# Performance work log

Hardware: AMD Instinct MI355X
Metric: run time of the kernel (lower is better)

The kernel has to match this reference:

```python
import jax, jax.numpy as jnp
import numpy as np

B, S, D, H = 4, 2048, 1024, 16
DK = D // H
NEG = -1e9


def setup_inputs() -> dict:
    key = jax.random.key(0)
    k1, k2, k3, k4 = jax.random.split(key, 4)
    x = jax.random.normal(k1, (B, S, D), dtype=jnp.float32)
    # seq_lens sorted descending; first entry must equal max_len (as the torch
    # code uses seq_lens[0] as max_len for the mask)
    sl = jax.random.randint(k2, (B,), S // 2, S + 1)
    sl = jnp.sort(sl)[::-1].at[0].set(S).astype(jnp.int64)
    # params of the output projection nn.Linear(d_m, d_m)
    lim = 1.0 / np.sqrt(D)
    W = jax.random.uniform(k3, (D, D), minval=-lim, maxval=lim, dtype=jnp.float32)
    b = jax.random.uniform(k4, (D,), minval=-lim, maxval=lim, dtype=jnp.float32)
    return {"x": x, "seq_lens": sl, "W": W, "b": b}


def reference(x, seq_lens, W, b):
    # key padding mask: (B, 1, 1, S) -> True where key position is valid
    valid = jnp.arange(S)[None, :] < seq_lens[:, None]          # (B, S)
    mask = valid[:, None, None, :]                              # (B, 1, 1, S)
    # split heads: (B, S, D) -> (B, H, S, DK)
    xh = x.reshape(B, S, H, DK).transpose(0, 2, 1, 3)
    scores = jnp.einsum("bhqd,bhkd->bhqk", xh, xh) / jnp.sqrt(jnp.float32(DK))
    scores = jnp.where(mask, scores, NEG)
    attn = jax.nn.softmax(scores, axis=-1)                      # (B, H, S, S)
    # dropout(0.1) omitted (eval-mode deterministic reference)
    ctx = jnp.einsum("bhqk,bhkd->bhqd", attn, xh)
    ctx = ctx.transpose(0, 2, 1, 3).reshape(B, S, D)
    out = ctx @ W.T + b                                         # (B, S, D)
    return (jnp.sum(out, axis=1), attn)
```

## Files before the change

### kernel.cpp

```cpp
#include <hip/hip_runtime.h>

#define S_  2048
#define D_  1024
#define H_  16
#define B_  4

typedef __attribute__((ext_vector_type(8))) short short8;
typedef __attribute__((ext_vector_type(4))) float f32x4;

__device__ __forceinline__ unsigned short f2bf(float f) {
  unsigned int u = __float_as_uint(f);
  u += 0x7fffu + ((u >> 16) & 1u);
  return (unsigned short)(u >> 16);
}
__device__ __forceinline__ unsigned int pack2(float a, float b) {
  return (unsigned int)f2bf(a) | ((unsigned int)f2bf(b) << 16);
}
__device__ __forceinline__ float h2f(unsigned int u, int shft) {
  unsigned short hs = (unsigned short)(u >> shft);
  return (float)__builtin_bit_cast(_Float16, hs);
}

#define SCL   0.18033688011112042f
#define EBIAS 12.0f

__global__ __launch_bounds__(256) void xcvt(const float* __restrict__ x,
                                            unsigned short* __restrict__ xh) {
  const int n = blockIdx.x;
  const int bh = n >> 5, chunk = n & 31;
  const int b = bh >> 4, h = bh & 15;
  const int r = threadIdx.x >> 2, cg = threadIdx.x & 3;
  const int srow = chunk * 64 + r;
  const float* src = x + ((size_t)b * S_ + srow) * D_ + h * 64 + cg * 16;
  float4 v0 = ((const float4*)src)[0];
  float4 v1 = ((const float4*)src)[1];
  float4 v2 = ((const float4*)src)[2];
  float4 v3 = ((const float4*)src)[3];
  uint4 w0, w1;
  w0.x = pack2(v0.x, v0.y); w0.y = pack2(v0.z, v0.w);
  w0.z = pack2(v1.x, v1.y); w0.w = pack2(v1.z, v1.w);
  w1.x = pack2(v2.x, v2.y); w1.y = pack2(v2.z, v2.w);
  w1.z = pack2(v3.x, v3.y); w1.w = pack2(v3.z, v3.w);
  unsigned short* dst = xh + ((size_t)bh * S_ + srow) * 64 + cg * 16;
  *(uint4*)dst = w0;
  *(uint4*)(dst + 8) = w1;
}

__global__ __launch_bounds__(256, 2) void attn_fused(
    const unsigned short* __restrict__ xh, const int* __restrict__ sl32,
    float* __restrict__ attn, unsigned int* __restrict__ cpart)
{
  __shared__ __align__(16) unsigned short kbuf[2][64 * 64];
  __shared__ __align__(16) unsigned int ebuf[8][2048];
  float* wbuf   = (float*)&kbuf[0][0];
  float* invbuf = (float*)&kbuf[1][0];

  const int n    = blockIdx.x;
  const int xcd  = n & 7;
  const int slot = n >> 3;
  const int bh   = (slot >> 7) * 8 + xcd;
  const int qt   = slot & 127;
  const int b    = bh >> 4;
  const int tid  = threadIdx.x;
  const int wv   = tid >> 6;
  const int lane = tid & 63;
  const int lo   = lane & 15;
  const int g    = lane >> 4;

  const bool is64 = (sl32[1] == 0);
  const int seqlen = is64 ? sl32[2 * b] : sl32[b];

  const unsigned short* xk = xh + (size_t)bh * S_ * 64;

  short8 aq0 = *(const short8*)(xk + (size_t)(qt * 16 + lo) * 64 + g * 8);
  short8 aq1 = *(const short8*)(xk + (size_t)(qt * 16 + lo) * 64 + g * 8 + 32);

  const int sr = tid >> 2, up = tid & 3;
  uint4 pf0, pf1;
  auto prefetch = [&](int c) {
    const uint4* src = (const uint4*)(xk + (size_t)(c * 64 + sr) * 64) + up * 2;
    pf0 = src[0]; pf1 = src[1];
  };
  auto commit = [&](unsigned short* dst) {
    uint4* d = (uint4*)&dst[sr * 64];
    const int sw = sr & 7;
    d[(up * 2) ^ sw]     = pf0;
    d[(up * 2 + 1) ^ sw] = pf1;
  };

  float rsum[4] = {0.f, 0.f, 0.f, 0.f};
  prefetch(0);
  commit(kbuf[0]);
  __syncthreads();
  const int lk = wv * 16 + lo;
  const int cs = g ^ (lk & 7);
  const int sA = ((g * 2) & 6) << 2;
  for (int c = 0; c < 32; ++c) {
    if (c < 31) prefetch(c + 1);
    const unsigned short* kb = kbuf[c & 1];
    short8 b0 = *(const short8*)&kb[lk * 64 + cs * 8];
    short8 b1 = *(const short8*)&kb[lk * 64 + (cs ^ 4) * 8];
    f32x4 acc = {0.f, 0.f, 0.f, 0.f};
    acc = __builtin_amdgcn_mfma_f32_16x16x32_bf16(aq0, b0, acc, 0, 0, 0);
    acc = __builtin_amdgcn_mfma_f32_16x16x32_bf16(aq1, b1, acc, 0, 0, 0);
    const int kg = c * 64 + lk;
    const bool valid = kg < seqlen;
    float e0 = valid ? exp2f(acc[0] * SCL - EBIAS) : 0.f;
    float e1 = valid ? exp2f(acc[1] * SCL - EBIAS) : 0.f;
    float e2 = valid ? exp2f(acc[2] * SCL - EBIAS) : 0.f;
    float e3 = valid ? exp2f(acc[3] * SCL - EBIAS) : 0.f;
    rsum[0] += e0; rsum[1] += e1; rsum[2] += e2; rsum[3] += e3;
    ebuf[g * 2][kg ^ sA] =
        __builtin_bit_cast(unsigned int, __builtin_amdgcn_cvt_pkrtz(e0, e1));
    ebuf[g * 2 + 1][kg ^ sA] =
        __builtin_bit_cast(unsigned int, __builtin_amdgcn_cvt_pkrtz(e2, e3));
    if (c < 31) commit(kbuf[(c + 1) & 1]);
    __syncthreads();
  }

#pragma unroll
  for (int r = 0; r < 4; ++r) {
    float v = rsum[r];
    v += __shfl_xor(v, 1);
    v += __shfl_xor(v, 2);
    v += __shfl_xor(v, 4);
    v += __shfl_xor(v, 8);
    if (lo == 0) wbuf[wv * 16 + g * 4 + r] = v;
  }
  __syncthreads();
  if (tid < 16)
    invbuf[tid] = 1.0f / (wbuf[tid] + wbuf[16 + tid] + wbuf[32 + tid] + wbuf[48 + tid]);
  __syncthreads();

  const int wr = tid >> 4, wc = tid & 15;
  const int r2w = wr >> 1, shw = (wr & 1) * 16, sw2 = (r2w & 6) << 2;
  const float vr = invbuf[wr];
  float* prow = attn + (size_t)bh * S_ * S_ + (size_t)(qt * 16 + wr) * S_;
#pragma unroll 8
  for (int i = 0; i < 32; ++i) {
    const int k0 = wc * 4 + i * 64;
    uint4 u = *(const uint4*)&ebuf[r2w][k0 ^ sw2];
    f32x4 v = {h2f(u.x, shw) * vr, h2f(u.y, shw) * vr,
               h2f(u.z, shw) * vr, h2f(u.w, shw) * vr};
    __builtin_nontemporal_store(v, (f32x4*)(prow + k0));
  }

  const int c0 = tid * 8;
  float a0 = 0.f, a1 = 0.f, a2 = 0.f, a3 = 0.f;
  float a4 = 0.f, a5 = 0.f, a6 = 0.f, a7 = 0.f;
#pragma unroll
  for (int r2 = 0; r2 < 8; ++r2) {
    const int s = (r2 & 6) << 2;
    const uint4 uA = *(const uint4*)&ebuf[r2][c0 ^ s];
    const uint4 uB = *(const uint4*)&ebuf[r2][(c0 ^ s) + 4];
    const float i0 = invbuf[2 * r2], i1 = invbuf[2 * r2 + 1];
    a0 += h2f(uA.x, 0) * i0 + h2f(uA.x, 16) * i1;
    a1 += h2f(uA.y, 0) * i0 + h2f(uA.y, 16) * i1;
    a2 += h2f(uA.z, 0) * i0 + h2f(uA.z, 16) * i1;
    a3 += h2f(uA.w, 0) * i0 + h2f(uA.w, 16) * i1;
    a4 += h2f(uB.x, 0) * i0 + h2f(uB.x, 16) * i1;
    a5 += h2f(uB.y, 0) * i0 + h2f(uB.y, 16) * i1;
    a6 += h2f(uB.z, 0) * i0 + h2f(uB.z, 16) * i1;
    a7 += h2f(uB.w, 0) * i0 + h2f(uB.w, 16) * i1;
  }
  uint4 w;
  w.x = __builtin_bit_cast(unsigned int, __builtin_amdgcn_cvt_pkrtz(a0, a1));
  w.y = __builtin_bit_cast(unsigned int, __builtin_amdgcn_cvt_pkrtz(a2, a3));
  w.z = __builtin_bit_cast(unsigned int, __builtin_amdgcn_cvt_pkrtz(a4, a5));
  w.w = __builtin_bit_cast(unsigned int, __builtin_amdgcn_cvt_pkrtz(a6, a7));
  *(uint4*)&cpart[(size_t)(bh * 128 + qt) * 1024 + tid * 4] = w;
}

__global__ __launch_bounds__(256) void csum2(const unsigned int* __restrict__ cpart,
                                             const unsigned short* __restrict__ xh,
                                             float* __restrict__ csump) {
  __shared__ float csh[256];
  __shared__ float part[4][64];
  const int bh = blockIdx.x >> 3, oct = blockIdx.x & 7;
  const int t = threadIdx.x;
  {
    const int k = oct * 256 + t;
    const unsigned short* cp =
        (const unsigned short*)cpart + (size_t)bh * 128 * 2048 + k;
    float s = 0.f;
#pragma unroll 8
    for (int q = 0; q < 128; ++q)
      s += (float)__builtin_bit_cast(_Float16, cp[(size_t)q * 2048]);
    csh[t] = s;
  }
  __syncthreads();
  const int seg = t >> 6, d = t & 63;
  const unsigned short* xb = xh + (size_t)bh * S_ * 64 + d;
  const int k0 = oct * 256 + seg * 64;
  float acc = 0.f;
#pragma unroll 4
  for (int kk = 0; kk < 64; ++kk) {
    float xv = __uint_as_float((unsigned int)xb[(size_t)(k0 + kk) * 64] << 16);
    acc += csh[seg * 64 + kk] * xv;
  }
  part[seg][d] = acc;
  __syncthreads();
  if (t < 64)
    csump[((size_t)oct * 64 + bh) * 64 + d] =
        part[0][d] + part[1][d] + part[2][d] + part[3][d];
}

__global__ __launch_bounds__(256) void proj_k(const float* __restrict__ csump,
                                              const float* __restrict__ W,
                                              const float* __restrict__ bias,
                                              float* __restrict__ out0) {
  const int idx = blockIdx.x * 4 + (threadIdx.x >> 6);
  const int b = idx >> 10, d = idx & 1023;
  const int lane = threadIdx.x & 63;
  const float* wr = W + (size_t)d * D_;
  float acc = 0.f;
#pragma unroll
  for (int e = 0; e < 16; ++e) {
    const int ei = lane + e * 64;
    const int bhh = b * 16 + (ei >> 6);
    const int dd = ei & 63;
    float cv = 0.f;
#pragma unroll
    for (int oct = 0; oct < 8; ++oct)
      cv += csump[((size_t)oct * 64 + bhh) * 64 + dd];
    acc += cv * wr[ei];
  }
  acc += __shfl_xor(acc, 32);
  acc += __shfl_xor(acc, 16);
  acc += __shfl_xor(acc, 8);
  acc += __shfl_xor(acc, 4);
  acc += __shfl_xor(acc, 2);
  acc += __shfl_xor(acc, 1);
  if (lane == 0) out0[idx] = acc + 2048.0f * bias[d];
}

extern "C" void kernel_launch(void* const* d_in, const int* in_sizes, int n_in,
                              void* d_out, int out_size, void* d_ws, size_t ws_size,
                              hipStream_t stream) {
  const float* x    = (const float*)d_in[0];
  const int*   sl   = (const int*)d_in[1];
  const float* W    = (const float*)d_in[2];
  const float* bias = (const float*)d_in[3];

  float* out0 = (float*)d_out;
  float* attn = out0 + B_ * D_;

  unsigned int* cpart = (unsigned int*)d_ws;
  float* csump = (float*)(cpart + (size_t)64 * 128 * 1024);
  unsigned short* xh = (unsigned short*)(csump + 8 * 64 * 64);

  hipLaunchKernelGGL(xcvt,       dim3(2048), dim3(256), 0, stream, x, xh);
  hipLaunchKernelGGL(attn_fused, dim3(8192), dim3(256), 0, stream, xh, sl, attn, cpart);
  hipLaunchKernelGGL(csum2,      dim3(512),  dim3(256), 0, stream, cpart, xh, csump);
  hipLaunchKernelGGL(proj_k,     dim3(1024), dim3(256), 0, stream, csump, W, bias, out0);
}
```

Before: 309.4 us.

## Make attention kernel persistent with producer/consumer warp specialization across query tiles

```diff
diff --git a/kernel.cpp b/kernel.cpp
--- a/kernel.cpp
+++ b/kernel.cpp
@@ -4,6 +4,7 @@
 #define D_  1024
 #define H_  16
 #define B_  4
+#define NT  32
 
 typedef __attribute__((ext_vector_type(8))) short short8;
 typedef __attribute__((ext_vector_type(4))) float f32x4;
@@ -19,6 +20,11 @@
 __device__ __forceinline__ float h2f(unsigned int u, int shft) {
   unsigned short hs = (unsigned short)(u >> shft);
   return (float)__builtin_bit_cast(_Float16, hs);
+}
+
+__device__ __forceinline__ void bar_lgkm() {
+  asm volatile("s_waitcnt lgkmcnt(0)" ::: "memory");
+  __builtin_amdgcn_s_barrier();
 }
 
 #define SCL   0.18033688011112042f
@@ -46,24 +52,26 @@
   *(uint4*)(dst + 8) = w1;
 }
 
-__global__ __launch_bounds__(256, 2) void attn_fused(
+__global__ __launch_bounds__(512, 1) void attn_fused(
     const unsigned short* __restrict__ xh, const int* __restrict__ sl32,
     float* __restrict__ attn, unsigned int* __restrict__ cpart)
 {
   __shared__ __align__(16) unsigned short kbuf[2][64 * 64];
-  __shared__ __align__(16) unsigned int ebuf[8][2048];
-  float* wbuf   = (float*)&kbuf[0][0];
-  float* invbuf = (float*)&kbuf[1][0];
+  __shared__ __align__(16) unsigned int ebuf[2][8][2048];
+  __shared__ float wbuf[64];
+  __shared__ float invbuf[2][16];
 
   const int n    = blockIdx.x;
   const int xcd  = n & 7;
-  const int slot = n >> 3;
-  const int bh   = (slot >> 7) * 8 + xcd;
-  const int qt   = slot & 127;
+  const int j    = n >> 3;
+  const int bh   = (j >> 2) * 8 + xcd;
+  const int q0   = (j & 3) * NT;
   const int b    = bh >> 4;
   const int tid  = threadIdx.x;
-  const int wv   = tid >> 6;
-  const int lane = tid & 63;
+  const int role = tid >> 8;
+  const int ctid = tid & 255;
+  const int cwv  = ctid >> 6;
+  const int lane = ctid & 63;
   const int lo   = lane & 15;
   const int g    = lane >> 4;
 
@@ -72,103 +80,145 @@
 
   const unsigned short* xk = xh + (size_t)bh * S_ * 64;
 
-  short8 aq0 = *(const short8*)(xk + (size_t)(qt * 16 + lo) * 64 + g * 8);
-  short8 aq1 = *(const short8*)(xk + (size_t)(qt * 16 + lo) * 64 + g * 8 + 32);
-
-  const int sr = tid >> 2, up = tid & 3;
-  uint4 pf0, pf1;
-  auto prefetch = [&](int c) {
+  const int sr = ctid >> 2, up = ctid & 3;
+  const int lk = cwv * 16 + lo;
+  const int cs = g ^ (lk & 7);
+  const int sA = ((g * 2) & 6) << 2;
+
+  const int wr = ctid >> 4, wc = ctid & 15;
+  const int r2w = wr >> 1, shw = (wr & 1) * 16, sw2 = (r2w & 6) << 2;
+
+  auto loadc = [&](int c, uint4& a, uint4& b2) {
     const uint4* src = (const uint4*)(xk + (size_t)(c * 64 + sr) * 64) + up * 2;
-    pf0 = src[0]; pf1 = src[1];
+    a = src[0]; b2 = src[1];
   };
-  auto commit = [&](unsigned short* dst) {
+  auto commitc = [&](unsigned short* dst, const uint4& a, const uint4& b2) {
     uint4* d = (uint4*)&dst[sr * 64];
     const int sw = sr & 7;
-    d[(up * 2) ^ sw]     = pf0;
-    d[(up * 2 + 1) ^ sw] = pf1;
+    d[(up * 2) ^ sw]     = a;
+    d[(up * 2 + 1) ^ sw] = b2;
   };
 
-  float rsum[4] = {0.f, 0.f, 0.f, 0.f};
-  prefetch(0);
-  commit(kbuf[0]);
-  __syncthreads();
-  const int lk = wv * 16 + lo;
-  const int cs = g ^ (lk & 7);
-  const int sA = ((g * 2) & 6) << 2;
-  for (int c = 0; c < 32; ++c) {
-    if (c < 31) prefetch(c + 1);
-    const unsigned short* kb = kbuf[c & 1];
-    short8 b0 = *(const short8*)&kb[lk * 64 + cs * 8];
-    short8 b1 = *(const short8*)&kb[lk * 64 + (cs ^ 4) * 8];
-    f32x4 acc = {0.f, 0.f, 0.f, 0.f};
-    acc = __builtin_amdgcn_mfma_f32_16x16x32_bf16(aq0, b0, acc, 0, 0, 0);
-    acc = __builtin_amdgcn_mfma_f32_16x16x32_bf16(aq1, b1, acc, 0, 0, 0);
-    const int kg = c * 64 + lk;
-    const bool valid = kg < seqlen;
-    float e0 = valid ? exp2f(acc[0] * SCL - EBIAS) : 0.f;
-    float e1 = valid ? exp2f(acc[1] * SCL - EBIAS) : 0.f;
-    float e2 = valid ? exp2f(acc[2] * SCL - EBIAS) : 0.f;
-    float e3 = valid ? exp2f(acc[3] * SCL - EBIAS) : 0.f;
-    rsum[0] += e0; rsum[1] += e1; rsum[2] += e2; rsum[3] += e3;
-    ebuf[g * 2][kg ^ sA] =
-        __builtin_bit_cast(unsigned int, __builtin_amdgcn_cvt_pkrtz(e0, e1));
-    ebuf[g * 2 + 1][kg ^ sA] =
-        __builtin_bit_cast(unsigned int, __builtin_amdgcn_cvt_pkrtz(e2, e3));
-    if (c < 31) commit(kbuf[(c + 1) & 1]);
-    __syncthreads();
+  uint4 pfE0, pfE1, pfO0, pfO1;
+  short8 aq0 = {}, aq1 = {};
+  float rsum0 = 0.f, rsum1 = 0.f, rsum2 = 0.f, rsum3 = 0.f;
+  float vr = 0.f;
+  float* prow = nullptr;
+
+  for (int ti = 0; ti <= NT; ++ti) {
+    unsigned int (*eb)[2048] = ebuf[ti & 1];
+    const unsigned int (*ebp)[2048] = ebuf[(ti + 1) & 1];
+
+    if (role == 0) {
+      if (ti < NT) {
+        const int qt = q0 + ti;
+        aq0 = *(const short8*)(xk + (size_t)(qt * 16 + lo) * 64 + g * 8);
+        aq1 = *(const short8*)(xk + (size_t)(qt * 16 + lo) * 64 + g * 8 + 32);
+        rsum0 = rsum1 = rsum2 = rsum3 = 0.f;
+        uint4 a, b2;
+        loadc(0, a, b2);
+        commitc(kbuf[0], a, b2);
+        loadc(1, pfO0, pfO1);
+      }
+    } else if (ti > 0) {
+      vr = invbuf[(ti - 1) & 1][wr];
+      prow = attn + (size_t)bh * S_ * S_ +
+             (size_t)((q0 + ti - 1) * 16 + wr) * S_;
+    }
+    bar_lgkm();
+
+    auto computec = [&](int c, const unsigned short* kb) {
+      short8 b0 = *(const short8*)&kb[lk * 64 + cs * 8];
+      short8 b1 = *(const short8*)&kb[lk * 64 + (cs ^ 4) * 8];
+      f32x4 acc = {0.f, 0.f, 0.f, 0.f};
+      acc = __builtin_amdgcn_mfma_f32_16x16x32_bf16(aq0, b0, acc, 0, 0, 0);
+      acc = __builtin_amdgcn_mfma_f32_16x16x32_bf16(aq1, b1, acc, 0, 0, 0);
+      const int kg = c * 64 + lk;
+      const bool valid = kg < seqlen;
+      float e0 = valid ? exp2f(acc[0] * SCL - EBIAS) : 0.f;
+      float e1 = valid ? exp2f(acc[1] * SCL - EBIAS) : 0.f;
+      float e2 = valid ? exp2f(acc[2] * SCL - EBIAS) : 0.f;
+      float e3 = valid ? exp2f(acc[3] * SCL - EBIAS) : 0.f;
+      rsum0 += e0; rsum1 += e1; rsum2 += e2; rsum3 += e3;
+      eb[g * 2][kg ^ sA] =
+          __builtin_bit_cast(unsigned int, __builtin_amdgcn_cvt_pkrtz(e0, e1));
+      eb[g * 2 + 1][kg ^ sA] =
+          __builtin_bit_cast(unsigned int, __builtin_amdgcn_cvt_pkrtz(e2, e3));
+    };
+    auto writec = [&](int r) {
+      const int k0 = wc * 4 + r * 64;
+      uint4 u = *(const uint4*)&ebp[r2w][k0 ^ sw2];
+      f32x4 v = {h2f(u.x, shw) * vr, h2f(u.y, shw) * vr,
+                 h2f(u.z, shw) * vr, h2f(u.w, shw) * vr};
+      __builtin_nontemporal_store(v, (f32x4*)(prow + k0));
+    };
+
+    for (int r = 0; r < 32; r += 2) {
+      if (role == 0) {
+        if (ti < NT) {
+          if (r + 2 < 32) loadc(r + 2, pfE0, pfE1);
+          computec(r, kbuf[0]);
+          commitc(kbuf[1], pfO0, pfO1);
+        }
+      } else if (ti > 0) writec(r);
+      bar_lgkm();
+      if (role == 0) {
+        if (ti < NT) {
+          if (r + 3 < 32) loadc(r + 3, pfO0, pfO1);
+          computec(r + 1, kbuf[1]);
+          if (r + 2 < 32) commitc(kbuf[0], pfE0, pfE1);
+        }
+      } else if (ti > 0) writec(r + 1);
+      bar_lgkm();
+    }
+
+    if (role == 0 && ti < NT) {
+      float rs[4] = {rsum0, rsum1, rsum2, rsum3};
+#pragma unroll
+      for (int r4 = 0; r4 < 4; ++r4) {
+        float v = rs[r4];
+        v += __shfl_xor(v, 1);
+        v += __shfl_xor(v, 2);
+        v += __shfl_xor(v, 4);
+        v += __shfl_xor(v, 8);
+        if (lo == 0) wbuf[cwv * 16 + g * 4 + r4] = v;
+      }
+    }
+    bar_lgkm();
+    if (role == 0) {
+      if (ti < NT && ctid < 16)
+        invbuf[ti & 1][ctid] = 1.0f / (wbuf[ctid] + wbuf[16 + ctid] +
+                                       wbuf[32 + ctid] + wbuf[48 + ctid]);
+      if (ti > 0) {
+        const float* ivp = invbuf[(ti - 1) & 1];
+        const int c0 = ctid * 8;
+        float a0 = 0.f, a1 = 0.f, a2 = 0.f, a3 = 0.f;
+        float a4 = 0.f, a5 = 0.f, a6 = 0.f, a7 = 0.f;
+#pragma unroll
+        for (int r2 = 0; r2 < 8; ++r2) {
+          const int s = (r2 & 6) << 2;
+          const uint4 uA = *(const uint4*)&ebp[r2][c0 ^ s];
+          const uint4 uB = *(const uint4*)&ebp[r2][(c0 ^ s) + 4];
+          const float i0 = ivp[2 * r2], i1 = ivp[2 * r2 + 1];
+          a0 += h2f(uA.x, 0) * i0 + h2f(uA.x, 16) * i1;
+          a1 += h2f(uA.y, 0) * i0 + h2f(uA.y, 16) * i1;
+          a2 += h2f(uA.z, 0) * i0 + h2f(uA.z, 16) * i1;
+          a3 += h2f(uA.w, 0) * i0 + h2f(uA.w, 16) * i1;
+          a4 += h2f(uB.x, 0) * i0 + h2f(uB.x, 16) * i1;
+          a5 += h2f(uB.y, 0) * i0 + h2f(uB.y, 16) * i1;
+          a6 += h2f(uB.z, 0) * i0 + h2f(uB.z, 16) * i1;
+          a7 += h2f(uB.w, 0) * i0 + h2f(uB.w, 16) * i1;
+        }
+        uint4 w;
+        w.x = __builtin_bit_cast(unsigned int, __builtin_amdgcn_cvt_pkrtz(a0, a1));
+        w.y = __builtin_bit_cast(unsigned int, __builtin_amdgcn_cvt_pkrtz(a2, a3));
+        w.z = __builtin_bit_cast(unsigned int, __builtin_amdgcn_cvt_pkrtz(a4, a5));
+        w.w = __builtin_bit_cast(unsigned int, __builtin_amdgcn_cvt_pkrtz(a6, a7));
+        *(uint4*)&cpart[(size_t)(bh * 128 + q0 + ti - 1) * 1024 + ctid * 4] = w;
+      }
+    }
+    bar_lgkm();
   }
-
-#pragma unroll
-  for (int r = 0; r < 4; ++r) {
-    float v = rsum[r];
-    v += __shfl_xor(v, 1);
-    v += __shfl_xor(v, 2);
-    v += __shfl_xor(v, 4);
-    v += __shfl_xor(v, 8);
-    if (lo == 0) wbuf[wv * 16 + g * 4 + r] = v;
-  }
-  __syncthreads();
-  if (tid < 16)
-    invbuf[tid] = 1.0f / (wbuf[tid] + wbuf[16 + tid] + wbuf[32 + tid] + wbuf[48 + tid]);
-  __syncthreads();
-
-  const int wr = tid >> 4, wc = tid & 15;
-  const int r2w = wr >> 1, shw = (wr & 1) * 16, sw2 = (r2w & 6) << 2;
-  const float vr = invbuf[wr];
-  float* prow = attn + (size_t)bh * S_ * S_ + (size_t)(qt * 16 + wr) * S_;
-#pragma unroll 8
-  for (int i = 0; i < 32; ++i) {
-    const int k0 = wc * 4 + i * 64;
-    uint4 u = *(const uint4*)&ebuf[r2w][k0 ^ sw2];
-    f32x4 v = {h2f(u.x, shw) * vr, h2f(u.y, shw) * vr,
-               h2f(u.z, shw) * vr, h2f(u.w, shw) * vr};
-    __builtin_nontemporal_store(v, (f32x4*)(prow + k0));
-  }
-
-  const int c0 = tid * 8;
-  float a0 = 0.f, a1 = 0.f, a2 = 0.f, a3 = 0.f;
-  float a4 = 0.f, a5 = 0.f, a6 = 0.f, a7 = 0.f;
-#pragma unroll
-  for (int r2 = 0; r2 < 8; ++r2) {
-    const int s = (r2 & 6) << 2;
-    const uint4 uA = *(const uint4*)&ebuf[r2][c0 ^ s];
-    const uint4 uB = *(const uint4*)&ebuf[r2][(c0 ^ s) + 4];
-    const float i0 = invbuf[2 * r2], i1 = invbuf[2 * r2 + 1];
-    a0 += h2f(uA.x, 0) * i0 + h2f(uA.x, 16) * i1;
-    a1 += h2f(uA.y, 0) * i0 + h2f(uA.y, 16) * i1;
-    a2 += h2f(uA.z, 0) * i0 + h2f(uA.z, 16) * i1;
-    a3 += h2f(uA.w, 0) * i0 + h2f(uA.w, 16) * i1;
-    a4 += h2f(uB.x, 0) * i0 + h2f(uB.x, 16) * i1;
-    a5 += h2f(uB.y, 0) * i0 + h2f(uB.y, 16) * i1;
-    a6 += h2f(uB.z, 0) * i0 + h2f(uB.z, 16) * i1;
-    a7 += h2f(uB.w, 0) * i0 + h2f(uB.w, 16) * i1;
-  }
-  uint4 w;
-  w.x = __builtin_bit_cast(unsigned int, __builtin_amdgcn_cvt_pkrtz(a0, a1));
-  w.y = __builtin_bit_cast(unsigned int, __builtin_amdgcn_cvt_pkrtz(a2, a3));
-  w.z = __builtin_bit_cast(unsigned int, __builtin_amdgcn_cvt_pkrtz(a4, a5));
-  w.w = __builtin_bit_cast(unsigned int, __builtin_amdgcn_cvt_pkrtz(a6, a7));
-  *(uint4*)&cpart[(size_t)(bh * 128 + qt) * 1024 + tid * 4] = w;
 }
 
 __global__ __launch_bounds__(256) void csum2(const unsigned int* __restrict__ cpart,
@@ -250,7 +300,7 @@
   unsigned short* xh = (unsigned short*)(csump + 8 * 64 * 64);
 
   hipLaunchKernelGGL(xcvt,       dim3(2048), dim3(256), 0, stream, x, xh);
-  hipLaunchKernelGGL(attn_fused, dim3(8192), dim3(256), 0, stream, xh, sl, attn, cpart);
+  hipLaunchKernelGGL(attn_fused, dim3(256),  dim3(512), 0, stream, xh, sl, attn, cpart);
   hipLaunchKernelGGL(csum2,      dim3(512),  dim3(256), 0, stream, cpart, xh, csump);
   hipLaunchKernelGGL(proj_k,     dim3(1024), dim3(256), 0, stream, csump, W, bias, out0);
 }
```

Result: slower. 583.4 us (+88.5%).

## Warp-specialize attention kernel into persistent producer/consumer pipeline over query tiles

Applied to the files above, without the earlier changes.

```diff
diff --git a/kernel.cpp b/kernel.cpp
--- a/kernel.cpp
+++ b/kernel.cpp
@@ -4,6 +4,7 @@
 #define D_  1024
 #define H_  16
 #define B_  4
+#define NT  32
 
 typedef __attribute__((ext_vector_type(8))) short short8;
 typedef __attribute__((ext_vector_type(4))) float f32x4;
@@ -46,23 +47,23 @@
   *(uint4*)(dst + 8) = w1;
 }
 
-__global__ __launch_bounds__(256, 2) void attn_fused(
+__global__ __launch_bounds__(768, 1) void attn_fused(
     const unsigned short* __restrict__ xh, const int* __restrict__ sl32,
     float* __restrict__ attn, unsigned int* __restrict__ cpart)
 {
-  __shared__ __align__(16) unsigned short kbuf[2][64 * 64];
-  __shared__ __align__(16) unsigned int ebuf[8][2048];
-  float* wbuf   = (float*)&kbuf[0][0];
-  float* invbuf = (float*)&kbuf[1][0];
+  __shared__ __align__(16) unsigned int ebuf[2][8][2048];
+  __shared__ float wbuf[128];
+  __shared__ float invbuf[2][16];
 
   const int n    = blockIdx.x;
   const int xcd  = n & 7;
-  const int slot = n >> 3;
-  const int bh   = (slot >> 7) * 8 + xcd;
-  const int qt   = slot & 127;
+  const int j    = n >> 3;
+  const int bh   = (j >> 2) * 8 + xcd;
+  const int q0   = (j & 3) * NT;
   const int b    = bh >> 4;
   const int tid  = threadIdx.x;
   const int wv   = tid >> 6;
+  const bool is_comp = wv < 8;
   const int lane = tid & 63;
   const int lo   = lane & 15;
   const int g    = lane >> 4;
@@ -72,103 +73,101 @@
 
   const unsigned short* xk = xh + (size_t)bh * S_ * 64;
 
-  short8 aq0 = *(const short8*)(xk + (size_t)(qt * 16 + lo) * 64 + g * 8);
-  short8 aq1 = *(const short8*)(xk + (size_t)(qt * 16 + lo) * 64 + g * 8 + 32);
-
-  const int sr = tid >> 2, up = tid & 3;
-  uint4 pf0, pf1;
-  auto prefetch = [&](int c) {
-    const uint4* src = (const uint4*)(xk + (size_t)(c * 64 + sr) * 64) + up * 2;
-    pf0 = src[0]; pf1 = src[1];
-  };
-  auto commit = [&](unsigned short* dst) {
-    uint4* d = (uint4*)&dst[sr * 64];
-    const int sw = sr & 7;
-    d[(up * 2) ^ sw]     = pf0;
-    d[(up * 2 + 1) ^ sw] = pf1;
-  };
-
-  float rsum[4] = {0.f, 0.f, 0.f, 0.f};
-  prefetch(0);
-  commit(kbuf[0]);
-  __syncthreads();
-  const int lk = wv * 16 + lo;
-  const int cs = g ^ (lk & 7);
   const int sA = ((g * 2) & 6) << 2;
-  for (int c = 0; c < 32; ++c) {
-    if (c < 31) prefetch(c + 1);
-    const unsigned short* kb = kbuf[c & 1];
-    short8 b0 = *(const short8*)&kb[lk * 64 + cs * 8];
-    short8 b1 = *(const short8*)&kb[lk * 64 + (cs ^ 4) * 8];
-    f32x4 acc = {0.f, 0.f, 0.f, 0.f};
-    acc = __builtin_amdgcn_mfma_f32_16x16x32_bf16(aq0, b0, acc, 0, 0, 0);
-    acc = __builtin_amdgcn_mfma_f32_16x16x32_bf16(aq1, b1, acc, 0, 0, 0);
-    const int kg = c * 64 + lk;
-    const bool valid = kg < seqlen;
-    float e0 = valid ? exp2f(acc[0] * SCL - EBIAS) : 0.f;
-    float e1 = valid ? exp2f(acc[1] * SCL - EBIAS) : 0.f;
-    float e2 = valid ? exp2f(acc[2] * SCL - EBIAS) : 0.f;
-    float e3 = valid ? exp2f(acc[3] * SCL - EBIAS) : 0.f;
-    rsum[0] += e0; rsum[1] += e1; rsum[2] += e2; rsum[3] += e3;
-    ebuf[g * 2][kg ^ sA] =
-        __builtin_bit_cast(unsigned int, __builtin_amdgcn_cvt_pkrtz(e0, e1));
-    ebuf[g * 2 + 1][kg ^ sA] =
-        __builtin_bit_cast(unsigned int, __builtin_amdgcn_cvt_pkrtz(e2, e3));
-    if (c < 31) commit(kbuf[(c + 1) & 1]);
+  const int wt  = tid & 255;
+  const int wr  = wt >> 4, wc = wt & 15;
+  const int r2w = wr >> 1, shw = (wr & 1) * 16, sw2 = (r2w & 6) << 2;
+
+  for (int ti = 0; ti <= NT; ++ti) {
+    unsigned int (*eb)[2048] = ebuf[ti & 1];
+    const unsigned int (*ebp)[2048] = ebuf[(ti + 1) & 1];
+
+    if (is_comp) {
+      if (ti < NT) {
+        const int qt = q0 + ti;
+        short8 aq0 = *(const short8*)(xk + (size_t)(qt * 16 + lo) * 64 + g * 8);
+        short8 aq1 = *(const short8*)(xk + (size_t)(qt * 16 + lo) * 64 + g * 8 + 32);
+        float r0 = 0.f, r1 = 0.f, r2s = 0.f, r3 = 0.f;
+#pragma unroll 4
+        for (int c = 0; c < 16; ++c) {
+          const int kt = c * 8 + wv;
+          const int kg = kt * 16 + lo;
+          const unsigned short* kp = xk + (size_t)kg * 64 + g * 8;
+          short8 b0 = *(const short8*)kp;
+          short8 b1 = *(const short8*)(kp + 32);
+          f32x4 acc = {0.f, 0.f, 0.f, 0.f};
+          acc = __builtin_amdgcn_mfma_f32_16x16x32_bf16(aq0, b0, acc, 0, 0, 0);
+          acc = __builtin_amdgcn_mfma_f32_16x16x32_bf16(aq1, b1, acc, 0, 0, 0);
+          const bool valid = kg < seqlen;
+          float e0 = valid ? exp2f(acc[0] * SCL - EBIAS) : 0.f;
+          float e1 = valid ? exp2f(acc[1] * SCL - EBIAS) : 0.f;
+          float e2 = valid ? exp2f(acc[2] * SCL - EBIAS) : 0.f;
+          float e3 = valid ? exp2f(acc[3] * SCL - EBIAS) : 0.f;
+          r0 += e0; r1 += e1; r2s += e2; r3 += e3;
+          eb[g * 2][kg ^ sA] =
+              __builtin_bit_cast(unsigned int, __builtin_amdgcn_cvt_pkrtz(e0, e1));
+          eb[g * 2 + 1][kg ^ sA] =
+              __builtin_bit_cast(unsigned int, __builtin_amdgcn_cvt_pkrtz(e2, e3));
+        }
+        float rs[4] = {r0, r1, r2s, r3};
+#pragma unroll
+        for (int r4 = 0; r4 < 4; ++r4) {
+          float v = rs[r4];
+          v += __shfl_xor(v, 1);
+          v += __shfl_xor(v, 2);
+          v += __shfl_xor(v, 4);
+          v += __shfl_xor(v, 8);
+          if (lo == 0) wbuf[wv * 16 + g * 4 + r4] = v;
+        }
+      }
+    } else if (ti > 0) {
+      const float* ivp = invbuf[(ti - 1) & 1];
+      const float vr = ivp[wr];
+      float* prow = attn + (size_t)bh * S_ * S_ +
+                    (size_t)((q0 + ti - 1) * 16 + wr) * S_;
+#pragma unroll 8
+      for (int i = 0; i < 32; ++i) {
+        const int k0 = wc * 4 + i * 64;
+        uint4 u = *(const uint4*)&ebp[r2w][k0 ^ sw2];
+        f32x4 v = {h2f(u.x, shw) * vr, h2f(u.y, shw) * vr,
+                   h2f(u.z, shw) * vr, h2f(u.w, shw) * vr};
+        __builtin_nontemporal_store(v, (f32x4*)(prow + k0));
+      }
+      const int c0 = wt * 8;
+      float a0 = 0.f, a1 = 0.f, a2 = 0.f, a3 = 0.f;
+      float a4 = 0.f, a5 = 0.f, a6 = 0.f, a7 = 0.f;
+#pragma unroll
+      for (int r2 = 0; r2 < 8; ++r2) {
+        const int s = (r2 & 6) << 2;
+        const uint4 uA = *(const uint4*)&ebp[r2][c0 ^ s];
+        const uint4 uB = *(const uint4*)&ebp[r2][(c0 ^ s) + 4];
+        const float i0 = ivp[2 * r2], i1 = ivp[2 * r2 + 1];
+        a0 += h2f(uA.x, 0) * i0 + h2f(uA.x, 16) * i1;
+        a1 += h2f(uA.y, 0) * i0 + h2f(uA.y, 16) * i1;
+        a2 += h2f(uA.z, 0) * i0 + h2f(uA.z, 16) * i1;
+        a3 += h2f(uA.w, 0) * i0 + h2f(uA.w, 16) * i1;
+        a4 += h2f(uB.x, 0) * i0 + h2f(uB.x, 16) * i1;
+        a5 += h2f(uB.y, 0) * i0 + h2f(uB.y, 16) * i1;
+        a6 += h2f(uB.z, 0) * i0 + h2f(uB.z, 16) * i1;
+        a7 += h2f(uB.w, 0) * i0 + h2f(uB.w, 16) * i1;
+      }
+      uint4 w;
+      w.x = __builtin_bit_cast(unsigned int, __builtin_amdgcn_cvt_pkrtz(a0, a1));
+      w.y = __builtin_bit_cast(unsigned int, __builtin_amdgcn_cvt_pkrtz(a2, a3));
+      w.z = __builtin_bit_cast(unsigned int, __builtin_amdgcn_cvt_pkrtz(a4, a5));
+      w.w = __builtin_bit_cast(unsigned int, __builtin_amdgcn_cvt_pkrtz(a6, a7));
+      *(uint4*)&cpart[(size_t)(bh * 128 + q0 + ti - 1) * 1024 + wt * 4] = w;
+    }
+
     __syncthreads();
-  }
-
-#pragma unroll
-  for (int r = 0; r < 4; ++r) {
-    float v = rsum[r];
-    v += __shfl_xor(v, 1);
-    v += __shfl_xor(v, 2);
-    v += __shfl_xor(v, 4);
-    v += __shfl_xor(v, 8);
-    if (lo == 0) wbuf[wv * 16 + g * 4 + r] = v;
-  }
-  __syncthreads();
-  if (tid < 16)
-    invbuf[tid] = 1.0f / (wbuf[tid] + wbuf[16 + tid] + wbuf[32 + tid] + wbuf[48 + tid]);
-  __syncthreads();
-
-  const int wr = tid >> 4, wc = tid & 15;
-  const int r2w = wr >> 1, shw = (wr & 1) * 16, sw2 = (r2w & 6) << 2;
-  const float vr = invbuf[wr];
-  float* prow = attn + (size_t)bh * S_ * S_ + (size_t)(qt * 16 + wr) * S_;
-#pragma unroll 8
-  for (int i = 0; i < 32; ++i) {
-    const int k0 = wc * 4 + i * 64;
-    uint4 u = *(const uint4*)&ebuf[r2w][k0 ^ sw2];
-    f32x4 v = {h2f(u.x, shw) * vr, h2f(u.y, shw) * vr,
-               h2f(u.z, shw) * vr, h2f(u.w, shw) * vr};
-    __builtin_nontemporal_store(v, (f32x4*)(prow + k0));
-  }
-
-  const int c0 = tid * 8;
-  float a0 = 0.f, a1 = 0.f, a2 = 0.f, a3 = 0.f;
-  float a4 = 0.f, a5 = 0.f, a6 = 0.f, a7 = 0.f;
-#pragma unroll
-  for (int r2 = 0; r2 < 8; ++r2) {
-    const int s = (r2 & 6) << 2;
-    const uint4 uA = *(const uint4*)&ebuf[r2][c0 ^ s];
-    const uint4 uB = *(const uint4*)&ebuf[r2][(c0 ^ s) + 4];
-    const float i0 = invbuf[2 * r2], i1 = invbuf[2 * r2 + 1];
-    a0 += h2f(uA.x, 0) * i0 + h2f(uA.x, 16) * i1;
-    a1 += h2f(uA.y, 0) * i0 + h2f(uA.y, 16) * i1;
-    a2 += h2f(uA.z, 0) * i0 + h2f(uA.z, 16) * i1;
-    a3 += h2f(uA.w, 0) * i0 + h2f(uA.w, 16) * i1;
-    a4 += h2f(uB.x, 0) * i0 + h2f(uB.x, 16) * i1;
-    a5 += h2f(uB.y, 0) * i0 + h2f(uB.y, 16) * i1;
-    a6 += h2f(uB.z, 0) * i0 + h2f(uB.z, 16) * i1;
-    a7 += h2f(uB.w, 0) * i0 + h2f(uB.w, 16) * i1;
-  }
-  uint4 w;
-  w.x = __builtin_bit_cast(unsigned int, __builtin_amdgcn_cvt_pkrtz(a0, a1));
-  w.y = __builtin_bit_cast(unsigned int, __builtin_amdgcn_cvt_pkrtz(a2, a3));
-  w.z = __builtin_bit_cast(unsigned int, __builtin_amdgcn_cvt_pkrtz(a4, a5));
-  w.w = __builtin_bit_cast(unsigned int, __builtin_amdgcn_cvt_pkrtz(a6, a7));
-  *(uint4*)&cpart[(size_t)(bh * 128 + qt) * 1024 + tid * 4] = w;
+    if (ti < NT && tid < 16) {
+      float s = 0.f;
+#pragma unroll
+      for (int w8 = 0; w8 < 8; ++w8) s += wbuf[w8 * 16 + tid];
+      invbuf[ti & 1][tid] = 1.0f / s;
+    }
+    __syncthreads();
+  }
 }
 
 __global__ __launch_bounds__(256) void csum2(const unsigned int* __restrict__ cpart,
@@ -250,7 +249,7 @@
   unsigned short* xh = (unsigned short*)(csump + 8 * 64 * 64);
 
   hipLaunchKernelGGL(xcvt,       dim3(2048), dim3(256), 0, stream, x, xh);
-  hipLaunchKernelGGL(attn_fused, dim3(8192), dim3(256), 0, stream, xh, sl, attn, cpart);
+  hipLaunchKernelGGL(attn_fused, dim3(256),  dim3(768), 0, stream, xh, sl, attn, cpart);
   hipLaunchKernelGGL(csum2,      dim3(512),  dim3(256), 0, stream, cpart, xh, csump);
   hipLaunchKernelGGL(proj_k,     dim3(1024), dim3(256), 0, stream, csump, W, bias, out0);
 }
```

Result: slower. 352.7 us (+14.0%).
